# Optimization experiments

Hardware: AMD Instinct MI355X
Metric: run time of the kernel (lower is better)

The kernel has to match this reference:

```python
import jax, jax.numpy as jnp
import numpy as np

H = 16        # GRU hidden / attn embed dim
EPS = 1e-5    # BatchNorm eps


def setup_inputs() -> dict:
    key = jax.random.key(0)
    ks = jax.random.split(key, 24)
    B, T = 32768, 50
    s = 0.1
    inp = {
        "user_id": jax.random.randint(ks[0], (B,), 0, 10000),
        "history_item_id": jax.random.randint(ks[1], (B, T), 0, 10000),
        "history_category_id": jax.random.randint(ks[2], (B, T), 0, 10),
        "target_item_id": jax.random.randint(ks[3], (B, 1), 0, 10000),
        "target_category_id": jax.random.randint(ks[4], (B, 1), 0, 10),
        # embedding tables
        "user_table": jax.random.normal(ks[5], (10000, 16)) * s,
        "item_table": jax.random.normal(ks[6], (10000, 12)) * s,
        "cat_table": jax.random.normal(ks[7], (10, 4)) * s,
        # GRU (torch layout: [3H, in], gates order r,z,n)
        "gru_Wih": jax.random.normal(ks[8], (3 * H, H)) * s,
        "gru_Whh": jax.random.normal(ks[9], (3 * H, H)) * s,
        "gru_bih": jax.random.normal(ks[10], (3 * H,)) * s,
        "gru_bhh": jax.random.normal(ks[11], (3 * H,)) * s,
        # MultiheadAttention, 1 head, embed 16 (in_proj packs q,k,v)
        "mha_Win": jax.random.normal(ks[12], (3 * H, H)) * s,
        "mha_bin": jax.random.normal(ks[13], (3 * H,)) * s,
        "mha_Wout": jax.random.normal(ks[14], (H, H)) * s,
        "mha_bout": jax.random.normal(ks[15], (H,)) * s,
        # BN(48) -> Linear(48,16) -> ReLU -> BN(16) -> Linear(16,2) -> Softmax
        "bn1_g": jnp.ones((48,)),
        "bn1_b": jnp.zeros((48,)),
        "fc1_W": jax.random.normal(ks[16], (16, 48)) * s,
        "fc1_b": jax.random.normal(ks[17], (16,)) * s,
        "bn2_g": jnp.ones((16,)),
        "bn2_b": jnp.zeros((16,)),
        "fc2_W": jax.random.normal(ks[18], (2, 16)) * s,
        "fc2_b": jax.random.normal(ks[19], (2,)) * s,
    }
    return inp


def _gru(x, Wih, Whh, bih, bhh):
    # x: [B, T, H] -> outputs [B, T, H]; torch GRU cell math
    xg = jnp.einsum("bti,gi->btg", x, Wih) + bih           # [B,T,3H]
    xg = jnp.moveaxis(xg, 1, 0)                             # [T,B,3H]
    h0 = jnp.zeros((x.shape[0], H), x.dtype)

    def step(h, xt):
        hg = h @ Whh.T + bhh                                # [B,3H]
        xr, xz, xn = jnp.split(xt, 3, axis=-1)
        hr, hz, hn = jnp.split(hg, 3, axis=-1)
        r = jax.nn.sigmoid(xr + hr)
        z = jax.nn.sigmoid(xz + hz)
        n = jnp.tanh(xn + r * hn)
        h = (1.0 - z) * n + z * h
        return h, h

    _, ys = jax.lax.scan(step, h0, xg)
    return jnp.moveaxis(ys, 0, 1)                           # [B,T,H]


def _mha(q_in, kv_in, Win, bin_, Wout, bout):
    # single-head attention, batch_first
    Wq, Wk, Wv = jnp.split(Win, 3, axis=0)
    bq, bk, bv = jnp.split(bin_, 3, axis=0)
    q = q_in @ Wq.T + bq                                    # [B,T,H]
    k = kv_in @ Wk.T + bk                                   # [B,S,H]
    v = kv_in @ Wv.T + bv                                   # [B,S,H]
    scores = jnp.einsum("btd,bsd->bts", q, k) / jnp.sqrt(jnp.asarray(H, q.dtype))
    attn = jax.nn.softmax(scores, axis=-1)
    ctx = jnp.einsum("bts,bsd->btd", attn, v)
    return ctx @ Wout.T + bout                              # [B,T,H]


def _bn(x, g, b):
    # training-mode BatchNorm1d over batch axis
    mu = x.mean(axis=0)
    var = x.var(axis=0)
    return (x - mu) * jax.lax.rsqrt(var + EPS) * g + b


def reference(user_id, history_item_id, history_category_id, target_item_id,
              target_category_id, user_table, item_table, cat_table,
              gru_Wih, gru_Whh, gru_bih, gru_bhh,
              mha_Win, mha_bin, mha_Wout, mha_bout,
              bn1_g, bn1_b, fc1_W, fc1_b, bn2_g, bn2_b, fc2_W, fc2_b):
    user_emb = user_table[user_id]                          # [B,16]
    hist_emb = jnp.concatenate(
        [item_table[history_item_id], cat_table[history_category_id]], axis=-1)  # [B,T,16]
    tgt_emb = jnp.concatenate(
        [item_table[target_item_id], cat_table[target_category_id]], axis=-1)    # [B,1,16]

    hist_enc = _gru(hist_emb, gru_Wih, gru_Whh, gru_bih, gru_bhh)                 # [B,T,16]
    attn = _mha(hist_enc, tgt_emb, mha_Win, mha_bin, mha_Wout, mha_bout)          # [B,T,16]
    avg = (attn * hist_enc).sum(axis=1)                                           # [B,16]

    all_enc = jnp.concatenate([avg, tgt_emb[:, 0, :], user_emb], axis=1)          # [B,48]
    h = _bn(all_enc, bn1_g, bn1_b)
    h = jax.nn.relu(h @ fc1_W.T + fc1_b)
    h = _bn(h, bn2_g, bn2_b)
    logits = h @ fc2_W.T + fc2_b
    return jax.nn.softmax(logits, axis=-1)                                        # [B,2]
```

## Files before the change

kernel.cpp:

```cpp
#include <hip/hip_runtime.h>

#define BN_EPS 1e-5f

typedef const float* fp;
typedef float f32x4 __attribute__((ext_vector_type(4)));
typedef _Float16 f16x2 __attribute__((ext_vector_type(2)));
typedef _Float16 f16x4 __attribute__((ext_vector_type(4)));
typedef _Float16 f16x8 __attribute__((ext_vector_type(8)));

__device__ __forceinline__ float frcp(float x) { return __builtin_amdgcn_rcpf(x); }
__device__ __forceinline__ float sigm(float x) { return frcp(1.0f + __expf(-x)); }
__device__ __forceinline__ float tanh_fast(float x) { return 1.0f - 2.0f * frcp(1.0f + __expf(2.0f * x)); }

__device__ __forceinline__ f32x4 ld4(const float* p) { return *(const f32x4*)p; }
__device__ __forceinline__ float dot4(f32x4 a, f32x4 b) {
    return a[0] * b[0] + a[1] * b[1] + a[2] * b[2] + a[3] * b[3];
}

#define MFMA32(A, B, C) __builtin_amdgcn_mfma_f32_16x16x32_f16((A), (B), (C), 0, 0, 0)

#define GLDS16(gp, lp) __builtin_amdgcn_global_load_lds( \
    (const __attribute__((address_space(1))) void*)(gp), \
    (__attribute__((address_space(3))) void*)(lp), 16, 0, 0)

__device__ __forceinline__ f16x4 pk_f16(f32x4 v) {
    f16x2 lo = __builtin_bit_cast(f16x2, __builtin_amdgcn_cvt_pkrtz(v[0], v[1]));
    f16x2 hi = __builtin_bit_cast(f16x2, __builtin_amdgcn_cvt_pkrtz(v[2], v[3]));
    return __builtin_shufflevector(lo, hi, 0, 1, 2, 3);
}

__global__ void k_zero(float* __restrict__ stats) { stats[threadIdx.x] = 0.f; }

__device__ __forceinline__ void gru_step_mf(
    f32x4 e4,
    const f16x8& Ar, const f16x8& ArL, const f16x8& Az, const f16x8& AzL,
    const f16x8& Anx, const f16x8& Anh,
    const f32x4& br4, const f32x4& bz4, const f32x4& bxn4, const f32x4& bhn4,
    f32x4& h, f32x4& hsum, f16x4& hh)
{
    f16x4 e_h = pk_f16(e4);
    f16x8 Bhh = __builtin_shufflevector(e_h, hh, 0, 1, 2, 3, 4, 5, 6, 7);
    f16x8 Bee = __builtin_shufflevector(e_h, e_h, 0, 1, 2, 3, 0, 1, 2, 3);
    f16x8 Bh2 = __builtin_shufflevector(hh, hh, 0, 1, 2, 3, 0, 1, 2, 3);
    f32x4 aR = MFMA32(Ar, Bhh, MFMA32(ArL, Bhh, br4));
    f32x4 aZ = MFMA32(Az, Bhh, MFMA32(AzL, Bhh, bz4));
    f32x4 xn = MFMA32(Anx, Bee, bxn4);
    f32x4 hn = MFMA32(Anh, Bh2, bhn4);
    f32x4 r, z, nv;
#pragma unroll
    for (int q = 0; q < 4; ++q) { r[q] = sigm(aR[q]); z[q] = sigm(aZ[q]); }
    f32x4 pre = r * hn + xn;
#pragma unroll
    for (int q = 0; q < 4; ++q) nv[q] = tanh_fast(pre[q]);
    h = z * (h - nv) + nv;
    hsum += h;
    hh = pk_f16(h);
}

__global__ __launch_bounds__(256, 2) void k_gru(
    const int* __restrict__ user_id, const int* __restrict__ hist_item,
    const int* __restrict__ hist_cat, const int* __restrict__ tgt_item,
    const int* __restrict__ tgt_cat,
    fp user_table, fp item_table, fp cat_table,
    fp Whh, fp bhh, fp Wih, fp bih,
    fp mha_Win, fp mha_bin, fp mha_Wout, fp mha_bout,
    float* __restrict__ all_enc, float* __restrict__ stats1, int B, int T)
{
    __shared__ float    s_stage[4][4][256];
    __shared__ unsigned s_ids[4][16 * 67];
    __shared__ float    lds_part[4][96];

    const int tid  = threadIdx.x;
    const int lane = tid & 63;
    const int wid  = tid >> 6;
    const int s    = lane & 15;
    const int hi   = lane >> 4;

    long b = (long)blockIdx.x * 64 + wid * 16 + s;
    const bool act = (b < B);
    if (!act) b = B - 1;

    const int ti  = tgt_item[b];
    const int tc  = tgt_cat[b];
    const int uid = user_id[b];
    asm volatile("" :: "v"(ti), "v"(tc), "v"(uid));

    {
        const int* ip = hist_item + b * T;
        const int* cp = hist_cat  + b * T;
        unsigned* d = &s_ids[wid][s * 67];
        for (int k = hi; k < T; k += 4)
            d[k] = (unsigned)ip[k] | ((unsigned)cp[k] << 16);
    }

    f32x4 wirf = ld4(&Wih[(0  + s) * 16 + 4 * hi]);
    f32x4 wizf = ld4(&Wih[(16 + s) * 16 + 4 * hi]);
    f32x4 winf = ld4(&Wih[(32 + s) * 16 + 4 * hi]);
    f32x4 whrf = ld4(&Whh[(0  + s) * 16 + 4 * hi]);
    f32x4 whzf = ld4(&Whh[(16 + s) * 16 + 4 * hi]);
    f32x4 whnf = ld4(&Whh[(32 + s) * 16 + 4 * hi]);
    f16x4 wir_h = __builtin_convertvector(wirf, f16x4);
    f16x4 wiz_h = __builtin_convertvector(wizf, f16x4);
    f16x4 win_h = __builtin_convertvector(winf, f16x4);
    f16x4 whr_h = __builtin_convertvector(whrf, f16x4);
    f16x4 whz_h = __builtin_convertvector(whzf, f16x4);
    f16x4 whn_h = __builtin_convertvector(whnf, f16x4);
    f16x4 wir_l = __builtin_convertvector(wirf - __builtin_convertvector(wir_h, f32x4), f16x4);
    f16x4 wiz_l = __builtin_convertvector(wizf - __builtin_convertvector(wiz_h, f32x4), f16x4);
    f16x4 win_l = __builtin_convertvector(winf - __builtin_convertvector(win_h, f32x4), f16x4);
    f16x4 whr_l = __builtin_convertvector(whrf - __builtin_convertvector(whr_h, f32x4), f16x4);
    f16x4 whz_l = __builtin_convertvector(whzf - __builtin_convertvector(whz_h, f32x4), f16x4);
    f16x4 whn_l = __builtin_convertvector(whnf - __builtin_convertvector(whn_h, f32x4), f16x4);
    f16x8 Ar  = __builtin_shufflevector(wir_h, whr_h, 0, 1, 2, 3, 4, 5, 6, 7);
    f16x8 ArL = __builtin_shufflevector(wir_l, whr_l, 0, 1, 2, 3, 4, 5, 6, 7);
    f16x8 Az  = __builtin_shufflevector(wiz_h, whz_h, 0, 1, 2, 3, 4, 5, 6, 7);
    f16x8 AzL = __builtin_shufflevector(wiz_l, whz_l, 0, 1, 2, 3, 4, 5, 6, 7);
    f16x8 Anx = __builtin_shufflevector(win_h, win_l, 0, 1, 2, 3, 4, 5, 6, 7);
    f16x8 Anh = __builtin_shufflevector(whn_h, whn_l, 0, 1, 2, 3, 4, 5, 6, 7);
    const f32x4 br4  = ld4(&bih[4 * hi])      + ld4(&bhh[4 * hi]);
    const f32x4 bz4  = ld4(&bih[16 + 4 * hi]) + ld4(&bhh[16 + 4 * hi]);
    const f32x4 bxn4 = ld4(&bih[32 + 4 * hi]);
    const f32x4 bhn4 = ld4(&bhh[32 + 4 * hi]);

    f32x4 h = {0.f, 0.f, 0.f, 0.f}, hsum = {0.f, 0.f, 0.f, 0.f};
    f16x4 hh = {};

    __syncthreads();

    const int T1 = T - 1;
    const unsigned* idsrow = &s_ids[wid][s * 67];
    float* stg = &s_stage[wid][0][0];
    const int l4 = lane * 4;

#define GADDR(pk) ((hi < 3) \
    ? (const char*)item_table + (size_t)((pk) & 0xffffu) * 48u + hi * 16 \
    : (const char*)cat_table  + (size_t)((pk) >> 16) * 16u)

    {
        unsigned p0 = idsrow[0];
        unsigned p1 = idsrow[(1 > T1) ? T1 : 1];
        unsigned p2 = idsrow[(2 > T1) ? T1 : 2];
        unsigned p3 = idsrow[(3 > T1) ? T1 : 3];
        GLDS16(GADDR(p0), stg);
        GLDS16(GADDR(p1), stg + 256);
        GLDS16(GADDR(p2), stg + 512);
        GLDS16(GADDR(p3), stg + 768);
    }
    unsigned idcdA = idsrow[(4 > T1) ? T1 : 4];
    asm volatile("s_waitcnt vmcnt(2)" ::: "memory");
    f32x4 eCur = ld4(stg + l4);

    for (int t = 0; t < T; ++t) {
        asm volatile("s_waitcnt vmcnt(2)" ::: "memory");
        asm volatile("s_waitcnt lgkmcnt(0)" ::: "memory");
        GLDS16(GADDR(idcdA), stg + ((t & 3) << 8));
        f32x4 eNext = ld4(stg + (((t + 1) & 3) << 8) + l4);
        int t5 = (t + 5 > T1) ? T1 : t + 5;
        unsigned idcdB = idsrow[t5];

        gru_step_mf(eCur, Ar, ArL, Az, AzL, Anx, Anh,
                    br4, bz4, bxn4, bhn4, h, hsum, hh);

        idcdA = idcdB;
        eCur  = eNext;
    }

    const float* itr = item_table + (size_t)ti * 12;
    f32x4 tv0 = ld4(itr), tv1 = ld4(itr + 4), tv2 = ld4(itr + 8);
    f32x4 tv3 = ld4(cat_table + tc * 4);

    f32x4 vq;
#pragma unroll
    for (int q = 0; q < 4; ++q) {
        int row = 32 + 4 * hi + q;
        const float* wv = mha_Win + row * 16;
        vq[q] = mha_bin[row] + dot4(ld4(wv), tv0) + dot4(ld4(wv + 4), tv1)
              + dot4(ld4(wv + 8), tv2) + dot4(ld4(wv + 12), tv3);
    }
    f32x4 vg0, vg1, vg2, vg3;
#pragma unroll
    for (int q = 0; q < 4; ++q) {
        vg0[q] = __shfl_xor(vq[q], (hi ^ 0) << 4);
        vg1[q] = __shfl_xor(vq[q], (hi ^ 1) << 4);
        vg2[q] = __shfl_xor(vq[q], (hi ^ 2) << 4);
        vg3[q] = __shfl_xor(vq[q], (hi ^ 3) << 4);
    }
    f32x4 aj;
#pragma unroll
    for (int q = 0; q < 4; ++q) {
        int row = 4 * hi + q;
        const float* wo = mha_Wout + row * 16;
        aj[q] = mha_bout[row] + dot4(ld4(wo), vg0) + dot4(ld4(wo + 4), vg1)
              + dot4(ld4(wo + 8), vg2) + dot4(ld4(wo + 12), vg3);
    }
    f32x4 avg = aj * hsum;

    f32x4 u4  = ld4(user_table + (size_t)uid * 16 + 4 * hi);
    f32x4 t4v = (hi == 0) ? tv0 : (hi == 1) ? tv1 : (hi == 2) ? tv2 : tv3;

    if (act) {
        float* er = all_enc + b * 48 + 4 * hi;
        *(f32x4*)er        = avg;
        *(f32x4*)(er + 16) = t4v;
        *(f32x4*)(er + 32) = u4;
    }

    const f32x4 zero4 = {0.f, 0.f, 0.f, 0.f};
    f32x4 sa = act ? avg : zero4, st = act ? t4v : zero4, su = act ? u4 : zero4;
    f32x4 qa = sa * sa, qt = st * st, qu = su * su;
#pragma unroll
    for (int m = 1; m <= 8; m <<= 1) {
#pragma unroll
        for (int q = 0; q < 4; ++q) {
            sa[q] += __shfl_xor(sa[q], m);
            st[q] += __shfl_xor(st[q], m);
            su[q] += __shfl_xor(su[q], m);
            qa[q] += __shfl_xor(qa[q], m);
            qt[q] += __shfl_xor(qt[q], m);
            qu[q] += __shfl_xor(qu[q], m);
        }
    }
    if (s == 0) {
        int c = 4 * hi;
#pragma unroll
        for (int q = 0; q < 4; ++q) {
            lds_part[wid][c + q]      = sa[q];
            lds_part[wid][16 + c + q] = st[q];
            lds_part[wid][32 + c + q] = su[q];
            lds_part[wid][48 + c + q] = qa[q];
            lds_part[wid][64 + c + q] = qt[q];
            lds_part[wid][80 + c + q] = qu[q];
        }
    }
    __syncthreads();
    if (tid < 96) {
        float v = lds_part[0][tid] + lds_part[1][tid] + lds_part[2][tid] + lds_part[3][tid];
        atomicAdd(&stats1[tid], v);
    }
}

__global__ __launch_bounds__(256) void k_fc1(
    const float* __restrict__ all_enc, const float* __restrict__ stats,
    fp fc1_W, fp fc1_b, fp g1, fp b1,
    float* __restrict__ hbuf, float* __restrict__ stats2, int B)
{
    const int tid = threadIdx.x, lane = tid & 63, wid = tid >> 6;
    const int j = lane & 15, sl = lane >> 4;
    __shared__ float kk[48], mm[48];
    __shared__ float part[4][32];

    if (tid < 48) {
        float mu  = stats[tid] / (float)B;
        float var = stats[48 + tid] / (float)B - mu * mu;
        float k   = rsqrtf(var + BN_EPS);
        float gk  = g1[tid] * k;
        kk[tid] = gk;
        mm[tid] = b1[tid] - mu * gk;
    }
    __syncthreads();

    float w[48];
    float bj = fc1_b[j];
#pragma unroll
    for (int q = 0; q < 12; ++q) {
        float4 v = *(const float4*)&fc1_W[j * 48 + q * 4];
        w[q * 4 + 0] = v.x * kk[q * 4 + 0];
        w[q * 4 + 1] = v.y * kk[q * 4 + 1];
        w[q * 4 + 2] = v.z * kk[q * 4 + 2];
        w[q * 4 + 3] = v.w * kk[q * 4 + 3];
        bj += v.x * mm[q * 4 + 0] + v.y * mm[q * 4 + 1]
            + v.z * mm[q * 4 + 2] + v.w * mm[q * 4 + 3];
    }

    float sh = 0.f, sq = 0.f;
    for (long b = (long)blockIdx.x * 16 + wid * 4 + sl; b < B; b += (long)gridDim.x * 16) {
        const float* x = all_enc + b * 48;
        float acc = bj;
#pragma unroll
        for (int q = 0; q < 12; ++q) {
            float4 v = *(const float4*)&x[q * 4];
            acc += w[q * 4] * v.x + w[q * 4 + 1] * v.y + w[q * 4 + 2] * v.z + w[q * 4 + 3] * v.w;
        }
        float h = fmaxf(acc, 0.f);
        hbuf[b * 16 + j] = h;
        sh += h; sq += h * h;
    }
    sh += __shfl_xor(sh, 16); sh += __shfl_xor(sh, 32);
    sq += __shfl_xor(sq, 16); sq += __shfl_xor(sq, 32);
    if (sl == 0) { part[wid][j] = sh; part[wid][16 + j] = sq; }
    __syncthreads();
    if (tid < 32) {
        float v = part[0][tid] + part[1][tid] + part[2][tid] + part[3][tid];
        atomicAdd(&stats2[tid], v);
    }
}

__global__ __launch_bounds__(256) void k_out(
    const float* __restrict__ hbuf, const float* __restrict__ stats2,
    fp fc2_W, fp fc2_b, fp g2, fp b2, float* __restrict__ out, int B)
{
    __shared__ float w[34];
    const int tid = threadIdx.x;
    if (tid < 32) {
        int c = tid & 15;
        float mu  = stats2[c] / (float)B;
        float var = stats2[16 + c] / (float)B - mu * mu;
        float gk  = g2[c] * rsqrtf(var + BN_EPS);
        w[tid] = fc2_W[tid] * gk;
    }
    if (tid < 2) {
        float acc = fc2_b[tid];
        for (int c = 0; c < 16; ++c) {
            float mu  = stats2[c] / (float)B;
            float var = stats2[16 + c] / (float)B - mu * mu;
            float gk  = g2[c] * rsqrtf(var + BN_EPS);
            acc += fc2_W[tid * 16 + c] * (b2[c] - mu * gk);
        }
        w[32 + tid] = acc;
    }
    __syncthreads();
    for (long b = (long)blockIdx.x * blockDim.x + threadIdx.x; b < B;
         b += (long)gridDim.x * blockDim.x) {
        const float* h = hbuf + b * 16;
        float l0 = w[32], l1 = w[33];
#pragma unroll
        for (int q = 0; q < 4; ++q) {
            float4 v = *(const float4*)&h[q * 4];
            l0 += w[q * 4] * v.x + w[q * 4 + 1] * v.y + w[q * 4 + 2] * v.z + w[q * 4 + 3] * v.w;
            l1 += w[16 + q * 4] * v.x + w[17 + q * 4] * v.y + w[18 + q * 4] * v.z + w[19 + q * 4] * v.w;
        }
        float m  = fmaxf(l0, l1);
        float e0 = __expf(l0 - m), e1 = __expf(l1 - m);
        float inv = frcp(e0 + e1);
        float2 p; p.x = e0 * inv; p.y = e1 * inv;
        *(float2*)&out[b * 2] = p;
    }
}

extern "C" void kernel_launch(void* const* d_in, const int* in_sizes, int n_in,
                              void* d_out, int out_size, void* d_ws, size_t ws_size,
                              hipStream_t stream)
{
    const int* user_id   = (const int*)d_in[0];
    const int* hist_item = (const int*)d_in[1];
    const int* hist_cat  = (const int*)d_in[2];
    const int* tgt_item  = (const int*)d_in[3];
    const int* tgt_cat   = (const int*)d_in[4];
    fp user_table = (fp)d_in[5];
    fp item_table = (fp)d_in[6];
    fp cat_table  = (fp)d_in[7];
    fp Wih = (fp)d_in[8],  Whh = (fp)d_in[9];
    fp bih = (fp)d_in[10], bhh = (fp)d_in[11];
    fp Win = (fp)d_in[12], binp = (fp)d_in[13];
    fp Wout = (fp)d_in[14], bout = (fp)d_in[15];
    fp g1 = (fp)d_in[16], b1 = (fp)d_in[17];
    fp fc1W = (fp)d_in[18], fc1b = (fp)d_in[19];
    fp g2 = (fp)d_in[20], b2 = (fp)d_in[21];
    fp fc2W = (fp)d_in[22], fc2b = (fp)d_in[23];

    const int B = in_sizes[0];
    const int T = in_sizes[1] / B;

    float* ws      = (float*)d_ws;
    float* stats   = ws;
    float* stats2  = stats + 96;
    float* all_enc = stats + 128;
    float* hbuf    = all_enc + (size_t)B * 48;

    hipLaunchKernelGGL(k_zero, dim3(1), dim3(128), 0, stream, stats);

    hipLaunchKernelGGL(k_gru, dim3((B + 63) / 64), dim3(256), 0, stream,
                       user_id, hist_item, hist_cat, tgt_item, tgt_cat,
                       user_table, item_table, cat_table, Whh, bhh, Wih, bih,
                       Win, binp, Wout, bout, all_enc, stats, B, T);

    hipLaunchKernelGGL(k_fc1, dim3(512), dim3(256), 0, stream,
                       all_enc, stats, fc1W, fc1b, g1, b1, hbuf, stats2, B);

    hipLaunchKernelGGL(k_out, dim3((B + 255) / 256), dim3(256), 0, stream,
                       hbuf, stats2, fc2W, fc2b, g2, b2, (float*)d_out, B);
}
```

Baseline: 68.35 us.

## Fuse fc1 and output kernels via grid barrier, keep hidden activations in registers

Result: slower. 97.13 us (+42.1%).

```diff
diff --git a/kernel.cpp b/kernel.cpp
--- a/kernel.cpp
+++ b/kernel.cpp
@@ -29,7 +29,9 @@
     return __builtin_shufflevector(lo, hi, 0, 1, 2, 3);
 }
 
-__global__ void k_zero(float* __restrict__ stats) { stats[threadIdx.x] = 0.f; }
+__global__ void k_zero(float* __restrict__ ws) {
+    if (threadIdx.x < 144) ws[threadIdx.x] = 0.f;
+}
 
 __device__ __forceinline__ void gru_step_mf(
     f32x4 e4,
@@ -132,9 +134,11 @@
     float* stg = &s_stage[wid][0][0];
     const int l4 = lane * 4;
 
-#define GADDR(pk) ((hi < 3) \
-    ? (const char*)item_table + (size_t)((pk) & 0xffffu) * 48u + hi * 16 \
-    : (const char*)cat_table  + (size_t)((pk) >> 16) * 16u)
+    const char*   gb   = (hi < 3) ? (const char*)item_table + hi * 16
+                                  : (const char*)cat_table;
+    const unsigned gsh  = (hi < 3) ? 0u : 16u;
+    const unsigned gmul = (hi < 3) ? 48u : 16u;
+#define GADDR(pk) (gb + (size_t)(((pk) >> gsh) & 0xffffu) * gmul)
 
     {
         unsigned p0 = idsrow[0];
@@ -151,8 +155,7 @@
     f32x4 eCur = ld4(stg + l4);
 
     for (int t = 0; t < T; ++t) {
-        asm volatile("s_waitcnt vmcnt(2)" ::: "memory");
-        asm volatile("s_waitcnt lgkmcnt(0)" ::: "memory");
+        asm volatile("s_waitcnt vmcnt(2) lgkmcnt(0)" ::: "memory");
         GLDS16(GADDR(idcdA), stg + ((t & 3) << 8));
         f32x4 eNext = ld4(stg + (((t + 1) & 3) << 8) + l4);
         int t5 = (t + 5 > T1) ? T1 : t + 5;
@@ -239,19 +242,22 @@
     }
 }
 
-__global__ __launch_bounds__(256) void k_fc1(
-    const float* __restrict__ all_enc, const float* __restrict__ stats,
+__global__ __launch_bounds__(256) void k_tail(
+    const float* __restrict__ all_enc, const float* __restrict__ stats1,
+    float* __restrict__ stats2, unsigned* __restrict__ ctr,
     fp fc1_W, fp fc1_b, fp g1, fp b1,
-    float* __restrict__ hbuf, float* __restrict__ stats2, int B)
+    fp fc2_W, fp fc2_b, fp g2, fp b2,
+    float* __restrict__ out, int B)
 {
     const int tid = threadIdx.x, lane = tid & 63, wid = tid >> 6;
     const int j = lane & 15, sl = lane >> 4;
     __shared__ float kk[48], mm[48];
     __shared__ float part[4][32];
+    __shared__ float sums2[32];
 
     if (tid < 48) {
-        float mu  = stats[tid] / (float)B;
-        float var = stats[48 + tid] / (float)B - mu * mu;
+        float mu  = stats1[tid] / (float)B;
+        float var = stats1[48 + tid] / (float)B - mu * mu;
         float k   = rsqrtf(var + BN_EPS);
         float gk  = g1[tid] * k;
         kk[tid] = gk;
@@ -272,18 +278,25 @@
             + v.z * mm[q * 4 + 2] + v.w * mm[q * 4 + 3];
     }
 
+    const long stride = (long)gridDim.x * 16;
+    const long b0 = (long)blockIdx.x * 16 + wid * 4 + sl;
+    float hv[4] = {0.f, 0.f, 0.f, 0.f};
     float sh = 0.f, sq = 0.f;
-    for (long b = (long)blockIdx.x * 16 + wid * 4 + sl; b < B; b += (long)gridDim.x * 16) {
-        const float* x = all_enc + b * 48;
-        float acc = bj;
-#pragma unroll
-        for (int q = 0; q < 12; ++q) {
-            float4 v = *(const float4*)&x[q * 4];
-            acc += w[q * 4] * v.x + w[q * 4 + 1] * v.y + w[q * 4 + 2] * v.z + w[q * 4 + 3] * v.w;
+#pragma unroll
+    for (int it = 0; it < 4; ++it) {
+        long b = b0 + it * stride;
+        if (b < B) {
+            const float* x = all_enc + b * 48;
+            float acc = bj;
+#pragma unroll
+            for (int q = 0; q < 12; ++q) {
+                float4 v = *(const float4*)&x[q * 4];
+                acc += w[q * 4] * v.x + w[q * 4 + 1] * v.y
+                     + w[q * 4 + 2] * v.z + w[q * 4 + 3] * v.w;
+            }
+            float h = fmaxf(acc, 0.f);
+            hv[it] = h; sh += h; sq += h * h;
         }
-        float h = fmaxf(acc, 0.f);
-        hbuf[b * 16 + j] = h;
-        sh += h; sq += h * h;
     }
     sh += __shfl_xor(sh, 16); sh += __shfl_xor(sh, 32);
     sq += __shfl_xor(sq, 16); sq += __shfl_xor(sq, 32);
@@ -293,47 +306,41 @@
         float v = part[0][tid] + part[1][tid] + part[2][tid] + part[3][tid];
         atomicAdd(&stats2[tid], v);
     }
-}
-
-__global__ __launch_bounds__(256) void k_out(
-    const float* __restrict__ hbuf, const float* __restrict__ stats2,
-    fp fc2_W, fp fc2_b, fp g2, fp b2, float* __restrict__ out, int B)
-{
-    __shared__ float w[34];
-    const int tid = threadIdx.x;
-    if (tid < 32) {
-        int c = tid & 15;
-        float mu  = stats2[c] / (float)B;
-        float var = stats2[16 + c] / (float)B - mu * mu;
-        float gk  = g2[c] * rsqrtf(var + BN_EPS);
-        w[tid] = fc2_W[tid] * gk;
-    }
-    if (tid < 2) {
-        float acc = fc2_b[tid];
-        for (int c = 0; c < 16; ++c) {
-            float mu  = stats2[c] / (float)B;
-            float var = stats2[16 + c] / (float)B - mu * mu;
-            float gk  = g2[c] * rsqrtf(var + BN_EPS);
-            acc += fc2_W[tid * 16 + c] * (b2[c] - mu * gk);
+    __syncthreads();
+
+    if (tid == 0) {
+        __threadfence();
+        atomicAdd(ctr, 1u);
+        while (atomicAdd(ctr, 0u) < gridDim.x) __builtin_amdgcn_s_sleep(2);
+    }
+    __syncthreads();
+    if (tid < 32) sums2[tid] = atomicAdd(&stats2[tid], 0.0f);
+    __syncthreads();
+
+    float mu2  = sums2[j] / (float)B;
+    float var2 = sums2[16 + j] / (float)B - mu2 * mu2;
+    float gk2  = g2[j] * rsqrtf(var2 + BN_EPS);
+    float mm2  = b2[j] - mu2 * gk2;
+    float w20 = fc2_W[j], w21 = fc2_W[16 + j];
+    float c0 = fc2_b[0], c1 = fc2_b[1];
+#pragma unroll
+    for (int it = 0; it < 4; ++it) {
+        long b = b0 + it * stride;
+        if (b >= B) continue;
+        float hbn = hv[it] * gk2 + mm2;
+        float v0 = w20 * hbn, v1 = w21 * hbn;
+        v0 += __shfl_xor(v0, 1); v1 += __shfl_xor(v1, 1);
+        v0 += __shfl_xor(v0, 2); v1 += __shfl_xor(v1, 2);
+        v0 += __shfl_xor(v0, 4); v1 += __shfl_xor(v1, 4);
+        v0 += __shfl_xor(v0, 8); v1 += __shfl_xor(v1, 8);
+        if (j == 0) {
+            float l0 = v0 + c0, l1 = v1 + c1;
+            float m  = fmaxf(l0, l1);
+            float e0 = __expf(l0 - m), e1 = __expf(l1 - m);
+            float inv = frcp(e0 + e1);
+            float2 p; p.x = e0 * inv; p.y = e1 * inv;
+            *(float2*)&out[b * 2] = p;
         }
-        w[32 + tid] = acc;
-    }
-    __syncthreads();
-    for (long b = (long)blockIdx.x * blockDim.x + threadIdx.x; b < B;
-         b += (long)gridDim.x * blockDim.x) {
-        const float* h = hbuf + b * 16;
-        float l0 = w[32], l1 = w[33];
-#pragma unroll
-        for (int q = 0; q < 4; ++q) {
-            float4 v = *(const float4*)&h[q * 4];
-            l0 += w[q * 4] * v.x + w[q * 4 + 1] * v.y + w[q * 4 + 2] * v.z + w[q * 4 + 3] * v.w;
-            l1 += w[16 + q * 4] * v.x + w[17 + q * 4] * v.y + w[18 + q * 4] * v.z + w[19 + q * 4] * v.w;
-        }
-        float m  = fmaxf(l0, l1);
-        float e0 = __expf(l0 - m), e1 = __expf(l1 - m);
-        float inv = frcp(e0 + e1);
-        float2 p; p.x = e0 * inv; p.y = e1 * inv;
-        *(float2*)&out[b * 2] = p;
     }
 }
 
@@ -361,22 +368,21 @@
     const int B = in_sizes[0];
     const int T = in_sizes[1] / B;
 
-    float* ws      = (float*)d_ws;
-    float* stats   = ws;
-    float* stats2  = stats + 96;
-    float* all_enc = stats + 128;
-    float* hbuf    = all_enc + (size_t)B * 48;
-
-    hipLaunchKernelGGL(k_zero, dim3(1), dim3(128), 0, stream, stats);
+    float* ws       = (float*)d_ws;
+    float* stats1   = ws;
+    float* stats2   = ws + 96;
+    unsigned* ctr   = (unsigned*)(ws + 128);
+    float* all_enc  = ws + 144;
+
+    hipLaunchKernelGGL(k_zero, dim3(1), dim3(256), 0, stream, ws);
 
     hipLaunchKernelGGL(k_gru, dim3((B + 63) / 64), dim3(256), 0, stream,
                        user_id, hist_item, hist_cat, tgt_item, tgt_cat,
                        user_table, item_table, cat_table, Whh, bhh, Wih, bih,
-                       Win, binp, Wout, bout, all_enc, stats, B, T);
-
-    hipLaunchKernelGGL(k_fc1, dim3(512), dim3(256), 0, stream,
-                       all_enc, stats, fc1W, fc1b, g1, b1, hbuf, stats2, B);
-
-    hipLaunchKernelGGL(k_out, dim3((B + 255) / 256), dim3(256), 0, stream,
-                       hbuf, stats2, fc2W, fc2b, g2, b2, (float*)d_out, B);
-}
+                       Win, binp, Wout, bout, all_enc, stats1, B, T);
+
+    hipLaunchKernelGGL(k_tail, dim3(512), dim3(256), 0, stream,
+                       all_enc, stats1, stats2, ctr,
+                       fc1W, fc1b, g1, b1, fc2W, fc2b, g2, b2,
+                       (float*)d_out, B);
+}
```
